# Kernel tuning notes

Measured on AMD Instinct MI355X. Metric: run time of the kernel, lower is better.

The kernel has to match this reference:

```python
import jax, jax.numpy as jnp
import numpy as np


def setup_inputs() -> dict:
    key = jax.random.key(0)
    ks = jax.random.split(key, 9)
    B, T, D, H = 64, 512, 512, 512
    inp = {
        "x": jax.random.normal(ks[0], (B, T, D), dtype=jnp.float32),
        "W_c": jax.random.normal(ks[1], (D, H), dtype=jnp.float32) * 0.02,
        "W_i": jax.random.normal(ks[2], (D, H), dtype=jnp.float32) * 0.02,
        "W_f": jax.random.normal(ks[3], (D, H), dtype=jnp.float32) * 0.02,
        "W_o": jax.random.normal(ks[4], (D, H), dtype=jnp.float32) * 0.02,
        "U_c": jax.random.normal(ks[5], (H, H), dtype=jnp.float32) * 0.02,
        "U_i": jax.random.normal(ks[6], (H, H), dtype=jnp.float32) * 0.02,
        "U_f": jax.random.normal(ks[7], (H, H), dtype=jnp.float32) * 0.02,
        "U_o": jax.random.normal(ks[8], (H, H), dtype=jnp.float32) * 0.02,
        "b_c": jnp.zeros((H,), dtype=jnp.float32),
        "b_i": jnp.zeros((H,), dtype=jnp.float32),
        "b_f": jnp.zeros((H,), dtype=jnp.float32),
        "b_o": jnp.zeros((H,), dtype=jnp.float32),
    }
    return inp


def reference(x, W_c, W_i, W_f, W_o, U_c, U_i, U_f, U_o, b_c, b_i, b_f, b_o):
    # x: [B, T, D] -> scan over time-major [T, B, D]
    B, T, D = x.shape
    H = W_c.shape[1]
    h0 = jnp.zeros((B, H), dtype=x.dtype)
    c0 = jnp.zeros((B, H), dtype=x.dtype)

    # Precompute input projections for all timesteps (same math, hoisted
    # out of the recurrence since x does not depend on state).
    xt = jnp.transpose(x, (1, 0, 2))  # [T, B, D]
    xa = jnp.einsum('tbd,dh->tbh', xt, W_c) + b_c
    xi = jnp.einsum('tbd,dh->tbh', xt, W_i) + b_i
    xf = jnp.einsum('tbd,dh->tbh', xt, W_f) + b_f
    xo = jnp.einsum('tbd,dh->tbh', xt, W_o) + b_o

    def step(carry, elems):
        h, c = carry
        xa_t, xi_t, xf_t, xo_t = elems
        a = jnp.tanh(xa_t + h @ U_c)
        i = jax.nn.sigmoid(xi_t + h @ U_i)
        f = jax.nn.sigmoid(xf_t + h @ U_f)
        o = jax.nn.sigmoid(xo_t + h @ U_o)
        c_new = i * a + f * c
        h_new = o * jnp.tanh(c_new)
        return (h_new, c_new), h_new

    _, hs = jax.lax.scan(step, (h0, c0), (xa, xi, xf, xo))  # hs: [T, B, H]
    return jnp.transpose(hs, (1, 0, 2))  # return_sequence=True -> [B, T, H]
```

## Files before the change

### kernel.cpp

```cpp
#include <hip/hip_runtime.h>
#include <cstdint>
#include <cstddef>

typedef _Float16 half8  __attribute__((ext_vector_type(8)));
typedef float    floatx4 __attribute__((ext_vector_type(4)));
typedef unsigned long long ull;

#define B_  64
#define T_  512
#define D_  512
#define H_  512

static __device__ __forceinline__ float fast_sigmoid(float x) {
  return 1.0f / (1.0f + __expf(-x));
}
static __device__ __forceinline__ float fast_tanh(float x) {
  x = fminf(15.0f, fmaxf(-15.0f, x));
  float e = __expf(2.0f * x);
  return (e - 1.0f) / (e + 1.0f);
}

#define LDS_BARRIER() do {                                   \
    asm volatile("s_waitcnt lgkmcnt(0)" ::: "memory");       \
    __builtin_amdgcn_s_barrier();                            \
  } while (0)

#define TAGMASK 0x0000FFFF0000FFFFull

__global__ __launch_bounds__(256) void scan_kernel(
    const float* __restrict__ x,
    const float* __restrict__ Wc, const float* __restrict__ Wi,
    const float* __restrict__ Wf, const float* __restrict__ Wo,
    const float* __restrict__ Uc, const float* __restrict__ Ui,
    const float* __restrict__ Uf, const float* __restrict__ Uo,
    const float* __restrict__ bc, const float* __restrict__ bi,
    const float* __restrict__ bf2, const float* __restrict__ bo,
    float* __restrict__ out, unsigned* __restrict__ dbuf)
{
  __shared__ _Float16 h_lds[16*640];
  __shared__ _Float16 xs_lds[16*640];

  int tid = threadIdx.x;
  int grp = blockIdx.x & 7;
  int member = blockIdx.x >> 3;

  int lane = tid & 63;
  int w    = tid >> 6;
  int c16  = lane & 15;
  int sub  = lane >> 4;
  int g    = c16 & 3;
  int jjl  = c16 >> 2;
  int jcol = member*16 + w*4 + jjl;
  int hi   = sub;
  bool pub = (g == 0) && (hi < 2);

  const float* Ug    = (g==0) ? Uc : (g==1) ? Ui : (g==2) ? Uf : Uo;
  const float* Wg    = (g==0) ? Wc : (g==1) ? Wi : (g==2) ? Wf : Wo;
  const float* biasg = (g==0) ? bc : (g==1) ? bi : (g==2) ? bf2 : bo;
  float bvs = biasg[jcol];

  half8 uf[16], wf[16];
  #pragma unroll
  for (int ks = 0; ks < 16; ++ks) {
    half8 vu, vw;
    #pragma unroll
    for (int q = 0; q < 8; ++q) {
      vu[q] = (_Float16)Ug[(size_t)(ks*32 + sub*8 + q) * H_ + jcol];
      vw[q] = (_Float16)Wg[(size_t)(ks*32 + sub*8 + q) * H_ + jcol];
    }
    uf[ks] = vu;
    wf[ks] = vw;
  }

  int sm  = tid >> 3;
  int sb  = tid & 7;
  _Float16* stg = &h_lds[(sm >> 1)*640 + sb*40 + (sm & 1)*16];

  const _Float16* abase = &h_lds[c16*40 + sub*8];
  const _Float16* pbase = &xs_lds[c16*40 + sub*8];

  int xr = tid >> 5;
  int xc = tid & 31;
  const float* xrow = x + (size_t)(grp*8 + xr) * T_ * D_ + (size_t)xc*16;
  _Float16* xstg = &xs_lds[(xc >> 1)*640 + xr*40 + (xc & 1)*16];

  float4 xr4[4];
  #define LD_X(tt) do {                                                   \
    const float4* p_ = (const float4*)(xrow + (size_t)(tt)*D_);           \
    xr4[0] = p_[0]; xr4[1] = p_[1]; xr4[2] = p_[2]; xr4[3] = p_[3];       \
  } while (0)
  #define ST_X() do {                                                     \
    half8 v0_, v1_;                                                       \
    v0_[0]=(_Float16)xr4[0].x; v0_[1]=(_Float16)xr4[0].y;                 \
    v0_[2]=(_Float16)xr4[0].z; v0_[3]=(_Float16)xr4[0].w;                 \
    v0_[4]=(_Float16)xr4[1].x; v0_[5]=(_Float16)xr4[1].y;                 \
    v0_[6]=(_Float16)xr4[1].z; v0_[7]=(_Float16)xr4[1].w;                 \
    v1_[0]=(_Float16)xr4[2].x; v1_[1]=(_Float16)xr4[2].y;                 \
    v1_[2]=(_Float16)xr4[2].z; v1_[3]=(_Float16)xr4[2].w;                 \
    v1_[4]=(_Float16)xr4[3].x; v1_[5]=(_Float16)xr4[3].y;                 \
    v1_[6]=(_Float16)xr4[3].z; v1_[7]=(_Float16)xr4[3].w;                 \
    *(half8*)xstg       = v0_;                                            \
    *(half8*)(xstg + 8) = v1_;                                            \
  } while (0)

  LD_X(0);
  ST_X();
  __syncthreads();
  float xgc[4];
  {
    floatx4 p0 = {bvs, bvs, bvs, bvs}, p1 = {0.f, 0.f, 0.f, 0.f};
    #pragma unroll
    for (int ks = 0; ks < 16; ks += 2) {
      half8 f0 = *(const half8*)(pbase + ks*640);
      p0 = __builtin_amdgcn_mfma_f32_16x16x32_f16(f0, wf[ks],   p0, 0, 0, 0);
      half8 f1 = *(const half8*)(pbase + (ks+1)*640);
      p1 = __builtin_amdgcn_mfma_f32_16x16x32_f16(f1, wf[ks+1], p1, 0, 0, 0);
    }
    #pragma unroll
    for (int i = 0; i < 4; ++i) xgc[i] = p0[i] + p1[i];
  }
  LD_X(1);

  floatx4 c4 = {0.f, 0.f, 0.f, 0.f};

  for (int t = 0; t < T_; ++t) {
    LDS_BARRIER();

    ST_X();

    {
      const ull* src8 = (const ull*)dbuf
          + ((size_t)(t & 1))*16384u + (size_t)grp*2048u + (size_t)tid*8u;
      ull want2 = (ull)(unsigned)(t & 0xFFFF) * 0x0000000100000001ull;
      ull w8[8];
      unsigned pend = 0xFFu;
      for (;;) {
        #pragma unroll
        for (int q = 0; q < 8; ++q)
          if (pend & (1u << q))
            w8[q] = __hip_atomic_load(src8 + q, __ATOMIC_RELAXED,
                                      __HIP_MEMORY_SCOPE_AGENT);
        unsigned npend = 0;
        #pragma unroll
        for (int q = 0; q < 8; ++q)
          if ((pend & (1u << q)) && ((w8[q] ^ want2) & TAGMASK))
            npend |= 1u << q;
        if (!npend) break;
        pend = npend;
        __builtin_amdgcn_s_sleep(2);
      }
      half8 hv0, hv1;
      #pragma unroll
      for (int q = 0; q < 4; ++q) {
        hv0[2*q]   = __builtin_bit_cast(_Float16, (unsigned short)((unsigned)w8[q]   >> 16));
        hv0[2*q+1] = __builtin_bit_cast(_Float16, (unsigned short)(w8[q]   >> 48));
        hv1[2*q]   = __builtin_bit_cast(_Float16, (unsigned short)((unsigned)w8[4+q] >> 16));
        hv1[2*q+1] = __builtin_bit_cast(_Float16, (unsigned short)(w8[4+q] >> 48));
      }
      *(half8*)stg       = hv0;
      *(half8*)(stg + 8) = hv1;
    }
    LDS_BARRIER();

    floatx4 a0 = {0.f,0.f,0.f,0.f}, a1 = {0.f,0.f,0.f,0.f};
    #pragma unroll
    for (int ks = 0; ks < 16; ks += 2) {
      half8 af0 = *(const half8*)(abase + ks*640);
      a0 = __builtin_amdgcn_mfma_f32_16x16x32_f16(af0, uf[ks],   a0, 0, 0, 0);
      half8 af1 = *(const half8*)(abase + (ks+1)*640);
      a1 = __builtin_amdgcn_mfma_f32_16x16x32_f16(af1, uf[ks+1], a1, 0, 0, 0);
    }

    float hval[4];
    #pragma unroll
    for (int i = 0; i < 4; ++i) {
      float pre = (a0[i] + a1[i]) + xgc[i];
      float act = (g == 0) ? fast_tanh(pre) : fast_sigmoid(pre);
      float t1  = __shfl_xor(act, 1);
      float ia  = act * t1;
      float fv  = __shfl_xor(act, 2);
      float ov  = __shfl_xor(t1, 2);
      float cn  = fmaf(fv, c4[i], ia);
      c4[i] = cn;
      float hv = ov * fast_tanh(cn);
      hval[i] = hv;
      if (pub && (t + 1 < T_)) {
        unsigned wv = ((unsigned)__builtin_bit_cast(unsigned short,
                            (_Float16)hv) << 16)
                    | ((unsigned)(t + 1) & 0xFFFFu);
        unsigned widx = ((unsigned)((t + 1) & 1))*32768u + (unsigned)grp*4096u
                      + (unsigned)member*128u
                      + (unsigned)((hi*4 + i)*16 + w*4 + jjl);
        __hip_atomic_store(&dbuf[widx], wv,
                           __ATOMIC_RELAXED, __HIP_MEMORY_SCOPE_AGENT);
      }
    }

    if (pub) {
      #pragma unroll
      for (int i = 0; i < 4; ++i)
        out[((size_t)(grp*8 + hi*4 + i) * T_ + t) * H_ + jcol] = hval[i];
    }

    {
      floatx4 p0 = {bvs, bvs, bvs, bvs}, p1 = {0.f, 0.f, 0.f, 0.f};
      #pragma unroll
      for (int ks = 0; ks < 16; ks += 2) {
        half8 f0 = *(const half8*)(pbase + ks*640);
        p0 = __builtin_amdgcn_mfma_f32_16x16x32_f16(f0, wf[ks],   p0, 0, 0, 0);
        half8 f1 = *(const half8*)(pbase + (ks+1)*640);
        p1 = __builtin_amdgcn_mfma_f32_16x16x32_f16(f1, wf[ks+1], p1, 0, 0, 0);
      }
      #pragma unroll
      for (int i = 0; i < 4; ++i) xgc[i] = p0[i] + p1[i];
    }

    {
      int xt = (t + 2 < T_) ? (t + 2) : (T_ - 1);
      LD_X(xt);
    }
  }
}

extern "C" void kernel_launch(void* const* d_in, const int* in_sizes, int n_in,
                              void* d_out, int out_size, void* d_ws, size_t ws_size,
                              hipStream_t stream)
{
  const float* x  = (const float*)d_in[0];
  const float* Wc = (const float*)d_in[1];
  const float* Wi = (const float*)d_in[2];
  const float* Wf = (const float*)d_in[3];
  const float* Wo = (const float*)d_in[4];
  const float* Uc = (const float*)d_in[5];
  const float* Ui = (const float*)d_in[6];
  const float* Uf = (const float*)d_in[7];
  const float* Uo = (const float*)d_in[8];
  const float* bc = (const float*)d_in[9];
  const float* bi = (const float*)d_in[10];
  const float* bf2= (const float*)d_in[11];
  const float* bo = (const float*)d_in[12];
  float* out = (float*)d_out;

  const size_t DB_BYTES = (size_t)2 * 8 * 4096 * sizeof(unsigned);

  if (ws_size < DB_BYTES) return;

  unsigned* dbuf = (unsigned*)d_ws;

  (void)hipMemsetAsync(dbuf, 0, DB_BYTES, stream);

  scan_kernel<<<dim3(256), dim3(256), 0, stream>>>(
      x, Wc, Wi, Wf, Wo, Uc, Ui, Uf, Uo, bc, bi, bf2, bo, out, dbuf);
}
```

Measured before the change: 2.253 ms.

## Overlap input projection MFMA with cross-block h polling via double-buffered x

Double-buffers the staged x tile in LDS and moves the next step's input-projection MFMA into the window between issuing the atomic loads of h and checking their tags. The aim is to hide the cross-workgroup synchronisation latency behind useful matrix work instead of doing the projection after the recurrent step. It also changes the LDS row stride from 640 to 648 halves, likely to reduce bank conflicts, and prefetches x one step further ahead. The cost is more LDS use and higher register pressure, and the scheduler barrier may constrain instruction scheduling.

```diff
diff --git a/kernel.cpp b/kernel.cpp
--- a/kernel.cpp
+++ b/kernel.cpp
@@ -10,6 +10,7 @@
 #define T_  512
 #define D_  512
 #define H_  512
+#define SKS 648
 
 static __device__ __forceinline__ float fast_sigmoid(float x) {
   return 1.0f / (1.0f + __expf(-x));
@@ -37,8 +38,9 @@
     const float* __restrict__ bf2, const float* __restrict__ bo,
     float* __restrict__ out, unsigned* __restrict__ dbuf)
 {
-  __shared__ _Float16 h_lds[16*640];
-  __shared__ _Float16 xs_lds[16*640];
+  __shared__ _Float16 h_lds[16*SKS];
+  __shared__ _Float16 xsA[16*SKS];
+  __shared__ _Float16 xsB[16*SKS];
 
   int tid = threadIdx.x;
   int grp = blockIdx.x & 7;
@@ -74,22 +76,22 @@
 
   int sm  = tid >> 3;
   int sb  = tid & 7;
-  _Float16* stg = &h_lds[(sm >> 1)*640 + sb*40 + (sm & 1)*16];
-
-  const _Float16* abase = &h_lds[c16*40 + sub*8];
-  const _Float16* pbase = &xs_lds[c16*40 + sub*8];
+  _Float16* stg = &h_lds[(sm >> 1)*SKS + sb*40 + (sm & 1)*16];
+
+  int fragoff = c16*40 + sub*8;
+  const _Float16* abase = &h_lds[fragoff];
 
   int xr = tid >> 5;
   int xc = tid & 31;
   const float* xrow = x + (size_t)(grp*8 + xr) * T_ * D_ + (size_t)xc*16;
-  _Float16* xstg = &xs_lds[(xc >> 1)*640 + xr*40 + (xc & 1)*16];
+  int xoff = (xc >> 1)*SKS + xr*40 + (xc & 1)*16;
 
   float4 xr4[4];
   #define LD_X(tt) do {                                                   \
     const float4* p_ = (const float4*)(xrow + (size_t)(tt)*D_);           \
     xr4[0] = p_[0]; xr4[1] = p_[1]; xr4[2] = p_[2]; xr4[3] = p_[3];       \
   } while (0)
-  #define ST_X() do {                                                     \
+  #define ST_X(dst_) do {                                                 \
     half8 v0_, v1_;                                                       \
     v0_[0]=(_Float16)xr4[0].x; v0_[1]=(_Float16)xr4[0].y;                 \
     v0_[2]=(_Float16)xr4[0].z; v0_[3]=(_Float16)xr4[0].w;                 \
@@ -99,42 +101,60 @@
     v1_[2]=(_Float16)xr4[2].z; v1_[3]=(_Float16)xr4[2].w;                 \
     v1_[4]=(_Float16)xr4[3].x; v1_[5]=(_Float16)xr4[3].y;                 \
     v1_[6]=(_Float16)xr4[3].z; v1_[7]=(_Float16)xr4[3].w;                 \
-    *(half8*)xstg       = v0_;                                            \
-    *(half8*)(xstg + 8) = v1_;                                            \
-  } while (0)
-
-  LD_X(0);
-  ST_X();
-  __syncthreads();
+    *(half8*)((dst_) + xoff)      = v0_;                                  \
+    *(half8*)((dst_) + xoff + 8)  = v1_;                                  \
+  } while (0)
+
+  #define PROJ_MFMA(src_, dst4_) do {                                    \
+    floatx4 p0_ = {bvs, bvs, bvs, bvs}, p1_ = {0.f, 0.f, 0.f, 0.f};      \
+    const _Float16* pb_ = (src_) + fragoff;                               \
+    _Pragma("unroll")                                                     \
+    for (int ks_ = 0; ks_ < 16; ks_ += 2) {                               \
+      half8 f0_ = *(const half8*)(pb_ + ks_*SKS);                         \
+      p0_ = __builtin_amdgcn_mfma_f32_16x16x32_f16(f0_, wf[ks_],   p0_, 0, 0, 0); \
+      half8 f1_ = *(const half8*)(pb_ + (ks_+1)*SKS);                     \
+      p1_ = __builtin_amdgcn_mfma_f32_16x16x32_f16(f1_, wf[ks_+1], p1_, 0, 0, 0); \
+    }                                                                     \
+    _Pragma("unroll")                                                     \
+    for (int i_ = 0; i_ < 4; ++i_) (dst4_)[i_] = p0_[i_] + p1_[i_];       \
+  } while (0)
+
+  LD_X(0);  ST_X(xsA);  __syncthreads();
   float xgc[4];
-  {
-    floatx4 p0 = {bvs, bvs, bvs, bvs}, p1 = {0.f, 0.f, 0.f, 0.f};
-    #pragma unroll
-    for (int ks = 0; ks < 16; ks += 2) {
-      half8 f0 = *(const half8*)(pbase + ks*640);
-      p0 = __builtin_amdgcn_mfma_f32_16x16x32_f16(f0, wf[ks],   p0, 0, 0, 0);
-      half8 f1 = *(const half8*)(pbase + (ks+1)*640);
-      p1 = __builtin_amdgcn_mfma_f32_16x16x32_f16(f1, wf[ks+1], p1, 0, 0, 0);
-    }
-    #pragma unroll
-    for (int i = 0; i < 4; ++i) xgc[i] = p0[i] + p1[i];
-  }
-  LD_X(1);
+  PROJ_MFMA(xsA, xgc);
+  LD_X(1);  ST_X(xsB);  __syncthreads();
+  LD_X(2);
 
   floatx4 c4 = {0.f, 0.f, 0.f, 0.f};
 
   for (int t = 0; t < T_; ++t) {
     LDS_BARRIER();
 
-    ST_X();
-
+    float xgn[4];
     {
       const ull* src8 = (const ull*)dbuf
           + ((size_t)(t & 1))*16384u + (size_t)grp*2048u + (size_t)tid*8u;
       ull want2 = (ull)(unsigned)(t & 0xFFFF) * 0x0000000100000001ull;
       ull w8[8];
-      unsigned pend = 0xFFu;
-      for (;;) {
+      #pragma unroll
+      for (int q = 0; q < 8; ++q)
+        w8[q] = __hip_atomic_load(src8 + q, __ATOMIC_RELAXED,
+                                  __HIP_MEMORY_SCOPE_AGENT);
+      __builtin_amdgcn_sched_barrier(0);
+
+      {
+        const _Float16* psrc = ((t + 1) & 1) ? xsB : xsA;
+        _Float16*       pdst = (t & 1) ? xsB : xsA;
+        PROJ_MFMA(psrc, xgn);
+        ST_X(pdst);
+      }
+
+      unsigned pend = 0;
+      #pragma unroll
+      for (int q = 0; q < 8; ++q)
+        if ((w8[q] ^ want2) & TAGMASK) pend |= 1u << q;
+      while (pend) {
+        __builtin_amdgcn_s_sleep(2);
         #pragma unroll
         for (int q = 0; q < 8; ++q)
           if (pend & (1u << q))
@@ -145,9 +165,7 @@
         for (int q = 0; q < 8; ++q)
           if ((pend & (1u << q)) && ((w8[q] ^ want2) & TAGMASK))
             npend |= 1u << q;
-        if (!npend) break;
         pend = npend;
-        __builtin_amdgcn_s_sleep(2);
       }
       half8 hv0, hv1;
       #pragma unroll
@@ -165,9 +183,9 @@
     floatx4 a0 = {0.f,0.f,0.f,0.f}, a1 = {0.f,0.f,0.f,0.f};
     #pragma unroll
     for (int ks = 0; ks < 16; ks += 2) {
-      half8 af0 = *(const half8*)(abase + ks*640);
+      half8 af0 = *(const half8*)(abase + ks*SKS);
       a0 = __builtin_amdgcn_mfma_f32_16x16x32_f16(af0, uf[ks],   a0, 0, 0, 0);
-      half8 af1 = *(const half8*)(abase + (ks+1)*640);
+      half8 af1 = *(const half8*)(abase + (ks+1)*SKS);
       a1 = __builtin_amdgcn_mfma_f32_16x16x32_f16(af1, uf[ks+1], a1, 0, 0, 0);
     }
 
@@ -202,21 +220,10 @@
         out[((size_t)(grp*8 + hi*4 + i) * T_ + t) * H_ + jcol] = hval[i];
     }
 
+    xgc[0] = xgn[0]; xgc[1] = xgn[1]; xgc[2] = xgn[2]; xgc[3] = xgn[3];
+
     {
-      floatx4 p0 = {bvs, bvs, bvs, bvs}, p1 = {0.f, 0.f, 0.f, 0.f};
-      #pragma unroll
-      for (int ks = 0; ks < 16; ks += 2) {
-        half8 f0 = *(const half8*)(pbase + ks*640);
-        p0 = __builtin_amdgcn_mfma_f32_16x16x32_f16(f0, wf[ks],   p0, 0, 0, 0);
-        half8 f1 = *(const half8*)(pbase + (ks+1)*640);
-        p1 = __builtin_amdgcn_mfma_f32_16x16x32_f16(f1, wf[ks+1], p1, 0, 0, 0);
-      }
-      #pragma unroll
-      for (int i = 0; i < 4; ++i) xgc[i] = p0[i] + p1[i];
-    }
-
-    {
-      int xt = (t + 2 < T_) ? (t + 2) : (T_ - 1);
+      int xt = (t + 3 < T_) ? (t + 3) : (T_ - 1);
       LD_X(xt);
     }
   }
```

Result: slower. 2.949 ms (+30.9%).
